# Optimization experiments

Hardware: AMD Instinct MI355X
Metric: run time of the kernel (lower is better)

## Reference

```python
import jax, jax.numpy as jnp
import numpy as np


def setup_inputs() -> dict:
    key = jax.random.key(0)
    kA, kB = jax.random.split(key)
    A = jax.random.normal(kA, (8, 256, 256, 64), dtype=jnp.float32)
    B = jax.random.normal(kB, (8, 256, 256, 64), dtype=jnp.float32)
    return {"A": A, "B": B}


def reference(A, B):
    # t-product: FFT along tube dim, batched complex matmul per frequency, IFFT.
    Af = jnp.fft.fft(A, axis=-1)          # [b, n1, n2, n3] complex
    Bf = jnp.fft.fft(B, axis=-1)          # [b, n2, n,  n3] complex
    # single batched complex GEMM over (b, n3) instead of a python loop
    Cf = jnp.einsum('bijk,bjnk->bink', Af, Bf)  # [b, n1, n, n3]
    C = jnp.fft.ifft(Cf, axis=-1)
    return jnp.real(C)
```

## Files before the change

kernel.cpp:

```cpp
#include <hip/hip_runtime.h>
#include <hip/hip_bf16.h>


typedef __bf16 bf16x8 __attribute__((ext_vector_type(8)));
typedef float f32x4 __attribute__((ext_vector_type(4)));

constexpr float TWC[32] = {
  1.0f, 0.99518472667f, 0.98078528040f, 0.95694033573f,
  0.92387953251f, 0.88192126435f, 0.83146961230f, 0.77301045336f,
  0.70710678119f, 0.63439328416f, 0.55557023302f, 0.47139673683f,
  0.38268343236f, 0.29028467725f, 0.19509032202f, 0.09801714033f,
  0.0f, -0.09801714033f, -0.19509032202f, -0.29028467725f,
  -0.38268343236f, -0.47139673683f, -0.55557023302f, -0.63439328416f,
  -0.70710678119f, -0.77301045336f, -0.83146961230f, -0.88192126435f,
  -0.92387953251f, -0.95694033573f, -0.98078528040f, -0.99518472667f
};
constexpr float TWS[32] = {
  0.0f, 0.09801714033f, 0.19509032202f, 0.29028467725f,
  0.38268343236f, 0.47139673683f, 0.55557023302f, 0.63439328416f,
  0.70710678119f, 0.77301045336f, 0.83146961230f, 0.88192126435f,
  0.92387953251f, 0.95694033573f, 0.98078528040f, 0.99518472667f,
  1.0f, 0.99518472667f, 0.98078528040f, 0.95694033573f,
  0.92387953251f, 0.88192126435f, 0.83146961230f, 0.77301045336f,
  0.70710678119f, 0.63439328416f, 0.55557023302f, 0.47139673683f,
  0.38268343236f, 0.29028467725f, 0.19509032202f, 0.09801714033f
};

__device__ __forceinline__ constexpr int rev6(int x) {
  int r = 0;
  for (int b = 0; b < 6; ++b) r = (r << 1) | ((x >> b) & 1);
  return r;
}

template <int SIGN>
__device__ __forceinline__ void fft64(float* re, float* im) {
#pragma unroll
  for (int i = 0; i < 64; ++i) {
    const int j = rev6(i);
    if (j > i) {
      float tr = re[i]; re[i] = re[j]; re[j] = tr;
      float ti = im[i]; im[i] = im[j]; im[j] = ti;
    }
  }
#pragma unroll
  for (int s = 0; s < 6; ++s) {
    const int half = 1 << s;
    const int m = 2 << s;
    const int tstep = 64 >> (s + 1);
#pragma unroll
    for (int kb = 0; kb < 64; kb += m) {
#pragma unroll
      for (int t = 0; t < half; ++t) {
        const int idx = t * tstep;
        const float wr = TWC[idx];
        const float wi = SIGN * TWS[idx];
        const int a = kb + t, b = a + half;
        const float xr = re[b] * wr - im[b] * wi;
        const float xi = re[b] * wi + im[b] * wr;
        re[b] = re[a] - xr; im[b] = im[a] - xi;
        re[a] += xr;        im[a] += xi;
      }
    }
  }
}

__global__ __launch_bounds__(64) void fft_a_kernel(const float* __restrict__ A,
                                                   __bf16* __restrict__ Af) {
  const int blk = blockIdx.x;
  const int jblk = blk & 3;
  const int bi = blk >> 2;
  const int lane = threadIdx.x;
  __shared__ float lds[64 * 65];
  const float* src = A + (((size_t)bi * 256) + (size_t)jblk * 64) * 64;
#pragma unroll
  for (int r = 0; r < 64; ++r) lds[r * 65 + lane] = src[(size_t)r * 64 + lane];
  __syncthreads();
  float re[64], im[64];
#pragma unroll
  for (int e = 0; e < 64; ++e) { re[e] = lds[lane * 65 + e]; im[e] = 0.0f; }
  fft64<-1>(re, im);
  const int b = bi >> 8, i = bi & 255;
  const int j = jblk * 64 + lane;
#pragma unroll
  for (int k = 0; k <= 32; ++k) {
    const size_t plane = (size_t)(b * 33 + k) * (256 * 512);
    Af[plane + (size_t)i * 512 + j]       = (__bf16)re[k];
    Af[plane + (size_t)i * 512 + 256 + j] = (__bf16)im[k];
  }
}

__global__ __launch_bounds__(64) void fft_b_kernel(const float* __restrict__ B,
                                                   __bf16* __restrict__ Bt) {
  const int blk = blockIdx.x;
  const int jblk = blk & 3;
  const int bn = blk >> 2;
  const int b = bn >> 8, n = bn & 255;
  const int lane = threadIdx.x;
  __shared__ float lds[64 * 65];
#pragma unroll
  for (int r = 0; r < 64; ++r) {
    const size_t base = (((size_t)b * 256 + (size_t)(jblk * 64 + r)) * 256 + n) * 64;
    lds[r * 65 + lane] = B[base + lane];
  }
  __syncthreads();
  float re[64], im[64];
#pragma unroll
  for (int e = 0; e < 64; ++e) { re[e] = lds[lane * 65 + e]; im[e] = 0.0f; }
  fft64<-1>(re, im);
  const int j = jblk * 64 + lane;
#pragma unroll
  for (int k = 0; k <= 32; ++k) {
    const size_t plane = (size_t)(b * 33 + k) * (512 * 512);
    const float br = re[k], bi = im[k];
    Bt[plane + (size_t)n * 512 + j]               = (__bf16)br;
    Bt[plane + (size_t)n * 512 + 256 + j]         = (__bf16)(-bi);
    Bt[plane + (size_t)(256 + n) * 512 + j]       = (__bf16)bi;
    Bt[plane + (size_t)(256 + n) * 512 + 256 + j] = (__bf16)br;
  }
}

__device__ __forceinline__ void gload_lds16(const void* g, void* l) {
  __builtin_amdgcn_global_load_lds(
      (const __attribute__((address_space(1))) void*)g,
      (__attribute__((address_space(3))) void*)l, 16, 0, 0);
}

__global__ __launch_bounds__(256) void gemm_kernel(const __bf16* __restrict__ Af,
                                                   const __bf16* __restrict__ Bt,
                                                   __bf16* __restrict__ Cf) {
  const int g = blockIdx.z;
  const int n0 = blockIdx.x * 128;
  const int i0 = blockIdx.y * 128;
  const int tid = threadIdx.x;
  const int lane = tid & 63, wv = tid >> 6;
  const int wm = wv >> 1, wn = wv & 1;
  const int lm = lane & 15, q = lane >> 4;

  __shared__ __bf16 As[128 * 64];
  __shared__ __bf16 Bs[128 * 64];

  const __bf16* aPlane = Af + (size_t)g * (256 * 512);
  const __bf16* bPlane = Bt + (size_t)g * (512 * 512);

  f32x4 acc[4][4];
#pragma unroll
  for (int mi = 0; mi < 4; ++mi)
#pragma unroll
    for (int ni = 0; ni < 4; ++ni) acc[mi][ni] = f32x4{0.f, 0.f, 0.f, 0.f};

  for (int kt = 0; kt < 8; ++kt) {
#pragma unroll
    for (int p = 0; p < 4; ++p) {
      const int row = p * 32 + wv * 8 + (lane >> 3);
      const int ke = (lane & 7) * 8;
      const __bf16* ga = aPlane + (size_t)(i0 + row) * 512 + kt * 64 + ke;
      const __bf16* gb = bPlane + (size_t)(n0 + row) * 512 + kt * 64 + ke;
      gload_lds16(ga, (char*)As + p * 4096 + wv * 1024);
      gload_lds16(gb, (char*)Bs + p * 4096 + wv * 1024);
    }
    __syncthreads();
#pragma unroll
    for (int ks = 0; ks < 2; ++ks) {
      bf16x8 af[4], bf[4];
#pragma unroll
      for (int mi = 0; mi < 4; ++mi)
        af[mi] = *(const bf16x8*)&As[(wm * 64 + mi * 16 + lm) * 64 + ks * 32 + q * 8];
#pragma unroll
      for (int ni = 0; ni < 4; ++ni)
        bf[ni] = *(const bf16x8*)&Bs[(wn * 64 + ni * 16 + lm) * 64 + ks * 32 + q * 8];
#pragma unroll
      for (int mi = 0; mi < 4; ++mi)
#pragma unroll
        for (int ni = 0; ni < 4; ++ni)
          acc[mi][ni] = __builtin_amdgcn_mfma_f32_16x16x32_bf16(af[mi], bf[ni],
                                                                acc[mi][ni], 0, 0, 0);
    }
    __syncthreads();
  }

  __bf16* cPlane = Cf + (size_t)g * (256 * 512);
#pragma unroll
  for (int mi = 0; mi < 4; ++mi) {
#pragma unroll
    for (int ni = 0; ni < 4; ++ni) {
      const int col = n0 + wn * 64 + ni * 16 + lm;
#pragma unroll
      for (int r = 0; r < 4; ++r) {
        const int row = i0 + wm * 64 + mi * 16 + q * 4 + r;
        cPlane[(size_t)row * 512 + col] = (__bf16)acc[mi][ni][r];
      }
    }
  }
}

__global__ __launch_bounds__(64) void ifft_kernel(const __bf16* __restrict__ Cf,
                                                  float* __restrict__ C) {
  const int blk = blockIdx.x;
  const int nblk = blk & 3;
  const int bi = blk >> 2;
  const int b = bi >> 8, i = bi & 255;
  const int lane = threadIdx.x;
  const int n = nblk * 64 + lane;
  float re[64], im[64];
#pragma unroll
  for (int k = 0; k <= 32; ++k) {
    const size_t plane = (size_t)(b * 33 + k) * (256 * 512);
    const float cr = (float)Cf[plane + (size_t)i * 512 + n];
    const float ci = (float)Cf[plane + (size_t)i * 512 + 256 + n];
    re[k] = cr; im[k] = ci;
    if (k >= 1 && k <= 31) { re[64 - k] = cr; im[64 - k] = -ci; }
  }
  fft64<1>(re, im);
  __shared__ float lds[64 * 65];
#pragma unroll
  for (int t = 0; t < 64; ++t) lds[lane * 65 + t] = re[t] * (1.0f / 64.0f);
  __syncthreads();
  const size_t base = (((size_t)b * 256 + i) * 256 + (size_t)nblk * 64) * 64;
#pragma unroll
  for (int r = 0; r < 64; ++r) C[base + (size_t)r * 64 + lane] = lds[r * 65 + lane];
}

extern "C" void kernel_launch(void* const* d_in, const int* in_sizes, int n_in,
                              void* d_out, int out_size, void* d_ws, size_t ws_size,
                              hipStream_t stream) {
  const float* A = (const float*)d_in[0];
  const float* B = (const float*)d_in[1];
  float* C = (float*)d_out;

  char* ws = (char*)d_ws;
  const size_t afBytes = (size_t)264 * 256 * 512 * 2;
  const size_t btBytes = (size_t)264 * 512 * 512 * 2;
  __bf16* Af = (__bf16*)ws;
  __bf16* Bt = (__bf16*)(ws + afBytes);
  __bf16* Cf = (__bf16*)(ws + afBytes + btBytes);

  fft_a_kernel<<<8192, 64, 0, stream>>>(A, Af);
  fft_b_kernel<<<8192, 64, 0, stream>>>(B, Bt);
  dim3 ggrid(4, 2, 264);
  gemm_kernel<<<ggrid, 256, 0, stream>>>(Af, Bt, Cf);
  ifft_kernel<<<8192, 64, 0, stream>>>(Cf, C);
}
```

Before: 462.5 us.

## Compute complex GEMM from separate real/imag B planes with sign-flip, swizzled LDS

The Bt layout that held the real-embedded 2x2 block form of B is dropped. B's real and imaginary planes are now stored once, and the complex product is formed in the GEMM with four MFMAs per tile, negating the imaginary operand by XOR-ing sign bits. This halves B's workspace size and the traffic to write and read it. LDS staging is restructured into four XOR-swizzled 32-wide slabs, and the grid is remapped to a flat index with launch bounds of 2 blocks per CU. The FFT kernels also switch to float4 global loads and stores through padded LDS. The cost is more accumulator registers, which may pressure occupancy.

```diff
diff --git a/kernel.cpp b/kernel.cpp
--- a/kernel.cpp
+++ b/kernel.cpp
@@ -1,5 +1,6 @@
 #include <hip/hip_runtime.h>
 #include <hip/hip_bf16.h>
+#include <stdint.h>
 
 
 typedef __bf16 bf16x8 __attribute__((ext_vector_type(8)));
@@ -69,18 +70,23 @@
   const int blk = blockIdx.x;
   const int jblk = blk & 3;
   const int bi = blk >> 2;
-  const int lane = threadIdx.x;
-  __shared__ float lds[64 * 65];
+  const int l = threadIdx.x;
+  const int lm16 = l & 15, lq4 = l >> 4;
+  __shared__ float lds[64 * 68];
   const float* src = A + (((size_t)bi * 256) + (size_t)jblk * 64) * 64;
 #pragma unroll
-  for (int r = 0; r < 64; ++r) lds[r * 65 + lane] = src[(size_t)r * 64 + lane];
+  for (int it = 0; it < 16; ++it) {
+    const int r = it * 4 + lq4;
+    const float4 v = *(const float4*)&src[(size_t)r * 64 + lm16 * 4];
+    *(float4*)&lds[r * 68 + lm16 * 4] = v;
+  }
   __syncthreads();
   float re[64], im[64];
 #pragma unroll
-  for (int e = 0; e < 64; ++e) { re[e] = lds[lane * 65 + e]; im[e] = 0.0f; }
+  for (int e = 0; e < 64; ++e) { re[e] = lds[l * 68 + e]; im[e] = 0.0f; }
   fft64<-1>(re, im);
   const int b = bi >> 8, i = bi & 255;
-  const int j = jblk * 64 + lane;
+  const int j = jblk * 64 + l;
 #pragma unroll
   for (int k = 0; k <= 32; ++k) {
     const size_t plane = (size_t)(b * 33 + k) * (256 * 512);
@@ -90,32 +96,32 @@
 }
 
 __global__ __launch_bounds__(64) void fft_b_kernel(const float* __restrict__ B,
-                                                   __bf16* __restrict__ Bt) {
+                                                   __bf16* __restrict__ Bn) {
   const int blk = blockIdx.x;
   const int jblk = blk & 3;
   const int bn = blk >> 2;
   const int b = bn >> 8, n = bn & 255;
-  const int lane = threadIdx.x;
-  __shared__ float lds[64 * 65];
-#pragma unroll
-  for (int r = 0; r < 64; ++r) {
+  const int l = threadIdx.x;
+  const int lm16 = l & 15, lq4 = l >> 4;
+  __shared__ float lds[64 * 68];
+#pragma unroll
+  for (int it = 0; it < 16; ++it) {
+    const int r = it * 4 + lq4;
     const size_t base = (((size_t)b * 256 + (size_t)(jblk * 64 + r)) * 256 + n) * 64;
-    lds[r * 65 + lane] = B[base + lane];
+    const float4 v = *(const float4*)&B[base + lm16 * 4];
+    *(float4*)&lds[r * 68 + lm16 * 4] = v;
   }
   __syncthreads();
   float re[64], im[64];
 #pragma unroll
-  for (int e = 0; e < 64; ++e) { re[e] = lds[lane * 65 + e]; im[e] = 0.0f; }
+  for (int e = 0; e < 64; ++e) { re[e] = lds[l * 68 + e]; im[e] = 0.0f; }
   fft64<-1>(re, im);
-  const int j = jblk * 64 + lane;
+  const int j = jblk * 64 + l;
 #pragma unroll
   for (int k = 0; k <= 32; ++k) {
-    const size_t plane = (size_t)(b * 33 + k) * (512 * 512);
-    const float br = re[k], bi = im[k];
-    Bt[plane + (size_t)n * 512 + j]               = (__bf16)br;
-    Bt[plane + (size_t)n * 512 + 256 + j]         = (__bf16)(-bi);
-    Bt[plane + (size_t)(256 + n) * 512 + j]       = (__bf16)bi;
-    Bt[plane + (size_t)(256 + n) * 512 + 256 + j] = (__bf16)br;
+    const size_t plane = (size_t)(b * 33 + k) * (256 * 512);
+    Bn[plane + (size_t)n * 512 + j]       = (__bf16)re[k];
+    Bn[plane + (size_t)n * 512 + 256 + j] = (__bf16)im[k];
   }
 }
 
@@ -125,72 +131,107 @@
       (__attribute__((address_space(3))) void*)l, 16, 0, 0);
 }
 
-__global__ __launch_bounds__(256) void gemm_kernel(const __bf16* __restrict__ Af,
-                                                   const __bf16* __restrict__ Bt,
-                                                   __bf16* __restrict__ Cf) {
-  const int g = blockIdx.z;
-  const int n0 = blockIdx.x * 128;
-  const int i0 = blockIdx.y * 128;
+__device__ __forceinline__ bf16x8 neg8(bf16x8 v) {
+  union { bf16x8 b; uint32_t u[4]; } x;
+  x.b = v;
+  x.u[0] ^= 0x80008000u; x.u[1] ^= 0x80008000u;
+  x.u[2] ^= 0x80008000u; x.u[3] ^= 0x80008000u;
+  return x.b;
+}
+
+__global__ __launch_bounds__(256, 2) void gemm_kernel(const __bf16* __restrict__ Af,
+                                                      const __bf16* __restrict__ Bn,
+                                                      __bf16* __restrict__ Cf) {
+  const int bid = blockIdx.x;
+  const int x = bid & 7, qx = bid >> 3;
+  const int g = x * 33 + (qx >> 2);
+  const int tile = qx & 3;
+  const int i0 = (tile >> 1) * 128, n0 = (tile & 1) * 128;
+
   const int tid = threadIdx.x;
   const int lane = tid & 63, wv = tid >> 6;
   const int wm = wv >> 1, wn = wv & 1;
-  const int lm = lane & 15, q = lane >> 4;
-
-  __shared__ __bf16 As[128 * 64];
-  __shared__ __bf16 Bs[128 * 64];
+  const int lm = lane & 15, qq = lane >> 4;
+
+  __shared__ __bf16 S[4][128 * 32];
 
   const __bf16* aPlane = Af + (size_t)g * (256 * 512);
-  const __bf16* bPlane = Bt + (size_t)g * (512 * 512);
-
-  f32x4 acc[4][4];
+  const __bf16* bPlane = Bn + (size_t)g * (256 * 512);
+
+  const int row_in = lane >> 2;
+  const int c_phys = lane & 3;
+  const int c_log = c_phys ^ ((row_in >> 1) & 3);
+  const __bf16* stageBase = (wv < 2 ? aPlane : bPlane);
+  const int r0 = (wv < 2 ? i0 : n0);
+  const int colOff = (wv & 1) * 256;
+  const __bf16* gsrc0 = stageBase + (size_t)(r0 + row_in) * 512 + colOff + c_log * 8;
+  char* ldst = (char*)&S[wv][0];
+
+  f32x4 acc_r[4][4], acc_i[4][4];
 #pragma unroll
   for (int mi = 0; mi < 4; ++mi)
 #pragma unroll
-    for (int ni = 0; ni < 4; ++ni) acc[mi][ni] = f32x4{0.f, 0.f, 0.f, 0.f};
+    for (int ni = 0; ni < 4; ++ni) {
+      acc_r[mi][ni] = f32x4{0.f, 0.f, 0.f, 0.f};
+      acc_i[mi][ni] = f32x4{0.f, 0.f, 0.f, 0.f};
+    }
+
+  int aoff[4], boff[4];
+#pragma unroll
+  for (int mi = 0; mi < 4; ++mi) {
+    const int R = wm * 64 + mi * 16 + lm;
+    aoff[mi] = R * 32 + ((qq ^ ((R >> 1) & 3)) * 8);
+  }
+#pragma unroll
+  for (int ni = 0; ni < 4; ++ni) {
+    const int R = wn * 64 + ni * 16 + lm;
+    boff[ni] = R * 32 + ((qq ^ ((R >> 1) & 3)) * 8);
+  }
 
   for (int kt = 0; kt < 8; ++kt) {
 #pragma unroll
-    for (int p = 0; p < 4; ++p) {
-      const int row = p * 32 + wv * 8 + (lane >> 3);
-      const int ke = (lane & 7) * 8;
-      const __bf16* ga = aPlane + (size_t)(i0 + row) * 512 + kt * 64 + ke;
-      const __bf16* gb = bPlane + (size_t)(n0 + row) * 512 + kt * 64 + ke;
-      gload_lds16(ga, (char*)As + p * 4096 + wv * 1024);
-      gload_lds16(gb, (char*)Bs + p * 4096 + wv * 1024);
+    for (int p = 0; p < 8; ++p) {
+      gload_lds16(gsrc0 + (size_t)p * 16 * 512 + kt * 32, ldst + p * 1024);
     }
     __syncthreads();
-#pragma unroll
-    for (int ks = 0; ks < 2; ++ks) {
-      bf16x8 af[4], bf[4];
-#pragma unroll
-      for (int mi = 0; mi < 4; ++mi)
-        af[mi] = *(const bf16x8*)&As[(wm * 64 + mi * 16 + lm) * 64 + ks * 32 + q * 8];
-#pragma unroll
-      for (int ni = 0; ni < 4; ++ni)
-        bf[ni] = *(const bf16x8*)&Bs[(wn * 64 + ni * 16 + lm) * 64 + ks * 32 + q * 8];
-#pragma unroll
-      for (int mi = 0; mi < 4; ++mi)
-#pragma unroll
-        for (int ni = 0; ni < 4; ++ni)
-          acc[mi][ni] = __builtin_amdgcn_mfma_f32_16x16x32_bf16(af[mi], bf[ni],
-                                                                acc[mi][ni], 0, 0, 0);
-    }
+
+    bf16x8 ar[4], ai[4], br[4], bi[4], nbi[4];
+#pragma unroll
+    for (int mi = 0; mi < 4; ++mi) {
+      ar[mi] = *(const bf16x8*)&S[0][aoff[mi]];
+      ai[mi] = *(const bf16x8*)&S[1][aoff[mi]];
+    }
+#pragma unroll
+    for (int ni = 0; ni < 4; ++ni) {
+      br[ni]  = *(const bf16x8*)&S[2][boff[ni]];
+      bi[ni]  = *(const bf16x8*)&S[3][boff[ni]];
+      nbi[ni] = neg8(bi[ni]);
+    }
+#pragma unroll
+    for (int mi = 0; mi < 4; ++mi)
+#pragma unroll
+      for (int ni = 0; ni < 4; ++ni) {
+        acc_r[mi][ni] = __builtin_amdgcn_mfma_f32_16x16x32_bf16(ar[mi], br[ni],  acc_r[mi][ni], 0, 0, 0);
+        acc_r[mi][ni] = __builtin_amdgcn_mfma_f32_16x16x32_bf16(ai[mi], nbi[ni], acc_r[mi][ni], 0, 0, 0);
+        acc_i[mi][ni] = __builtin_amdgcn_mfma_f32_16x16x32_bf16(ar[mi], bi[ni],  acc_i[mi][ni], 0, 0, 0);
+        acc_i[mi][ni] = __builtin_amdgcn_mfma_f32_16x16x32_bf16(ai[mi], br[ni],  acc_i[mi][ni], 0, 0, 0);
+      }
     __syncthreads();
   }
 
   __bf16* cPlane = Cf + (size_t)g * (256 * 512);
 #pragma unroll
-  for (int mi = 0; mi < 4; ++mi) {
+  for (int mi = 0; mi < 4; ++mi)
 #pragma unroll
     for (int ni = 0; ni < 4; ++ni) {
       const int col = n0 + wn * 64 + ni * 16 + lm;
 #pragma unroll
       for (int r = 0; r < 4; ++r) {
-        const int row = i0 + wm * 64 + mi * 16 + q * 4 + r;
-        cPlane[(size_t)row * 512 + col] = (__bf16)acc[mi][ni][r];
+        const int row = i0 + wm * 64 + mi * 16 + qq * 4 + r;
+        cPlane[(size_t)row * 512 + col]       = (__bf16)acc_r[mi][ni][r];
+        cPlane[(size_t)row * 512 + 256 + col] = (__bf16)acc_i[mi][ni][r];
       }
     }
-  }
 }
 
 __global__ __launch_bounds__(64) void ifft_kernel(const __bf16* __restrict__ Cf,
@@ -199,8 +240,9 @@
   const int nblk = blk & 3;
   const int bi = blk >> 2;
   const int b = bi >> 8, i = bi & 255;
-  const int lane = threadIdx.x;
-  const int n = nblk * 64 + lane;
+  const int l = threadIdx.x;
+  const int lm16 = l & 15, lq4 = l >> 4;
+  const int n = nblk * 64 + l;
   float re[64], im[64];
 #pragma unroll
   for (int k = 0; k <= 32; ++k) {
@@ -211,13 +253,17 @@
     if (k >= 1 && k <= 31) { re[64 - k] = cr; im[64 - k] = -ci; }
   }
   fft64<1>(re, im);
-  __shared__ float lds[64 * 65];
-#pragma unroll
-  for (int t = 0; t < 64; ++t) lds[lane * 65 + t] = re[t] * (1.0f / 64.0f);
+  __shared__ float lds[64 * 68];
+#pragma unroll
+  for (int t = 0; t < 64; ++t) lds[l * 68 + t] = re[t] * (1.0f / 64.0f);
   __syncthreads();
   const size_t base = (((size_t)b * 256 + i) * 256 + (size_t)nblk * 64) * 64;
 #pragma unroll
-  for (int r = 0; r < 64; ++r) C[base + (size_t)r * 64 + lane] = lds[r * 65 + lane];
+  for (int it = 0; it < 16; ++it) {
+    const int r = it * 4 + lq4;
+    const float4 v = *(const float4*)&lds[r * 68 + lm16 * 4];
+    *(float4*)&C[base + (size_t)r * 64 + lm16 * 4] = v;
+  }
 }
 
 extern "C" void kernel_launch(void* const* d_in, const int* in_sizes, int n_in,
@@ -228,15 +274,13 @@
   float* C = (float*)d_out;
 
   char* ws = (char*)d_ws;
-  const size_t afBytes = (size_t)264 * 256 * 512 * 2;
-  const size_t btBytes = (size_t)264 * 512 * 512 * 2;
+  const size_t planeBytes = (size_t)264 * 256 * 512 * 2;
   __bf16* Af = (__bf16*)ws;
-  __bf16* Bt = (__bf16*)(ws + afBytes);
-  __bf16* Cf = (__bf16*)(ws + afBytes + btBytes);
+  __bf16* Bn = (__bf16*)(ws + planeBytes);
+  __bf16* Cf = (__bf16*)(ws + 2 * planeBytes);
 
   fft_a_kernel<<<8192, 64, 0, stream>>>(A, Af);
-  fft_b_kernel<<<8192, 64, 0, stream>>>(B, Bt);
-  dim3 ggrid(4, 2, 264);
-  gemm_kernel<<<ggrid, 256, 0, stream>>>(Af, Bt, Cf);
+  fft_b_kernel<<<8192, 64, 0, stream>>>(B, Bn);
+  gemm_kernel<<<1056, 256, 0, stream>>>(Af, Bn, Cf);
   ifft_kernel<<<8192, 64, 0, stream>>>(Cf, C);
 }
```

Result: faster. 419.0 us (-9.4%).
